# Optimization experiments

Measured on AMD Instinct MI355X. Metric: run time of the kernel, lower is better.

Reference implementation:

```python
import jax, jax.numpy as jnp
import numpy as np

B, S, H = 8, 4096, 2048
E, F, K = 32, 128, 2
UTIL_BONUS = 0.1
CAP_PENALTY = 0.1


def setup_inputs() -> dict:
    key = jax.random.key(0)
    ks = jax.random.split(key, 4)
    hidden = jax.random.normal(ks[0], (B, S, H), dtype=jnp.float32)
    router_w = 0.02 * jax.random.normal(ks[1], (E, H), dtype=jnp.float32)
    router_b = jnp.zeros((E,), dtype=jnp.float32)
    w1 = 0.02 * jax.random.normal(ks[2], (E, F, H), dtype=jnp.float32)
    b1 = jnp.zeros((E, F), dtype=jnp.float32)
    w2 = 0.02 * jax.random.normal(ks[3], (E, H, F), dtype=jnp.float32)
    b2 = jnp.zeros((E, H), dtype=jnp.float32)
    activation_counts = jnp.zeros((E,), dtype=jnp.float32)
    expert_drift = jnp.zeros((E,), dtype=jnp.float32)
    return {"hidden": hidden, "router_w": router_w, "router_b": router_b,
            "w1": w1, "b1": b1, "w2": w2, "b2": b2,
            "activation_counts": activation_counts, "expert_drift": expert_drift}


def reference(hidden, router_w, router_b, w1, b1, w2, b2, activation_counts, expert_drift):
    # --- router with usage bonus / capacity penalty (buffers are zero at init) ---
    pooled = hidden.mean(axis=1)                      # [B, H]
    base_logits = pooled @ router_w.T + router_b      # [B, E]
    total = activation_counts.sum()
    usage = activation_counts / jnp.maximum(total, 1e-8)
    bonus = jnp.where(total > 0.0, UTIL_BONUS * (1.0 - usage), jnp.zeros_like(usage))
    usage_norm = activation_counts / jnp.maximum(activation_counts.max(), 1e-8)
    drift_norm = expert_drift / jnp.maximum(expert_drift.max(), 1e-8)
    penalty = CAP_PENALTY * 0.5 * (usage_norm + drift_norm)
    logits = base_logits + bonus[None, :] - penalty[None, :]
    router_probs = jax.nn.softmax(logits, axis=-1)    # [B, E]

    topk_probs, topk_idx = jax.lax.top_k(router_probs, K)  # [B, K]
    topk_probs = topk_probs / jnp.maximum(topk_probs.sum(axis=-1, keepdims=True), 1e-8)

    # --- gather selected expert weights and apply to the full sequence ---
    W1 = w1[topk_idx]   # [B, K, F, H]
    B1 = b1[topk_idx]   # [B, K, F]
    W2 = w2[topk_idx]   # [B, K, H, F]
    B2 = b2[topk_idx]   # [B, K, H]

    h1 = jnp.einsum('bsh,bkfh->bksf', hidden, W1) + B1[:, :, None, :]
    h1 = jax.nn.gelu(h1, approximate=False)           # torch nn.GELU default = exact erf
    out = jnp.einsum('bksf,bkhf->bksh', h1, W2) + B2[:, :, None, :]
    delta = jnp.einsum('bk,bksh->bsh', topk_probs, out)  # weighted combine
    return delta, topk_idx, topk_probs, router_probs
```

## Files before the change

### kernel.cpp

```cpp
#include <hip/hip_runtime.h>
#include <hip/hip_bf16.h>

#define BB 8
#define SS 4096
#define HH 2048
#define EE 32
#define FF 128

constexpr size_t DELTA_N = (size_t)BB * SS * HH;
constexpr size_t WELEM = (size_t)EE * FF * HH;
constexpr size_t WBYTES = WELEM * 2;
constexpr size_t HB16_BYTES = (size_t)BB * SS * HH * 2;

typedef short bf16x8 __attribute__((ext_vector_type(8)));
typedef float f32x4 __attribute__((ext_vector_type(4)));
typedef unsigned short u16;
typedef __attribute__((address_space(3))) unsigned char as3u8;
typedef __attribute__((address_space(1))) const unsigned char as1u8;

#define WAITV(N)                                             \
  do {                                                       \
    asm volatile("s_waitcnt vmcnt(" #N ")" ::: "memory");    \
    __builtin_amdgcn_sched_barrier(0);                       \
  } while (0)
#define BARRIER()                                            \
  do {                                                       \
    __builtin_amdgcn_s_barrier();                            \
    __builtin_amdgcn_sched_barrier(0);                       \
  } while (0)

__device__ __forceinline__ u16 f2bfu(float x) {
  unsigned int u = __float_as_uint(x);
  u = (u + 0x7FFFu + ((u >> 16) & 1u)) >> 16;
  return (u16)u;
}

__device__ __forceinline__ unsigned int pk2(float a, float b) {
  union { __hip_bfloat162 h; unsigned int u; } c;
  c.h = __float22bfloat162_rn(make_float2(a, b));
  return c.u;
}

__device__ __forceinline__ bf16x8 pack8(float4 a, float4 b) {
  union { bf16x8 v; unsigned int u[4]; } r;
  r.u[0] = pk2(a.x, a.y);
  r.u[1] = pk2(a.z, a.w);
  r.u[2] = pk2(b.x, b.y);
  r.u[3] = pk2(b.z, b.w);
  return r.v;
}

__device__ __forceinline__ void glds16(const void* g, void* l) {
  __builtin_amdgcn_global_load_lds((as1u8*)g, (as3u8*)l, 16, 0, 0);
}

__global__ void k_zero(float* __restrict__ ws, int n) {
  int i = blockIdx.x * 256 + threadIdx.x;
  if (i < n) ws[i] = 0.0f;
}

__global__ void k_pack(const float* __restrict__ w1, const float* __restrict__ w2,
                       u16* __restrict__ w1p, u16* __restrict__ w2p) {
  unsigned c = blockIdx.x * 256 + threadIdx.x;
  const float* src;
  u16* dst;
  if (c < 1048576u) {
    unsigned e = c >> 15, ci = c & 32767u;
    unsigned it = ci >> 10;
    unsigned cb = (ci & 1023u) * 16u;
    unsigned col = cb >> 7;
    unsigned kb = (cb & 127u) ^ ((col & 7u) << 4);
    unsigned k = it * 64u + (kb >> 1);
    src = w1 + ((size_t)(e * 128u + col) * HH + k);
    dst = w1p + (size_t)c * 8;
  } else {
    unsigned c2 = c - 1048576u;
    unsigned e = c2 >> 15, ci = c2 & 32767u;
    unsigned h = ci >> 4;
    unsigned cb = (ci & 15u) * 16u;
    unsigned kb = cb ^ ((h & 7u) << 4);
    unsigned f = kb >> 1;
    src = w2 + ((size_t)(e * 2048u + h) * FF + f);
    dst = w2p + (size_t)c2 * 8;
  }
  float4 a = *(const float4*)src;
  float4 b = *(const float4*)(src + 4);
  *(bf16x8*)dst = pack8(a, b);
}

__global__ __launch_bounds__(512) void k_pooltile(const float* __restrict__ hidden,
                                                  u16* __restrict__ hb16,
                                                  float* __restrict__ psum) {
  const int b  = blockIdx.x >> 6;
  const int st = blockIdx.x & 63;
  const int t  = threadIdx.x;

  const float* src = hidden + ((size_t)b * SS + st * 64) * HH + t * 4;
  char* dbase = (char*)hb16 + (size_t)(b * 64 + st) * 262144 + (size_t)(t >> 4) * 8192;
  const int kq = (t & 15) * 8;

  float4 s = make_float4(0.f, 0.f, 0.f, 0.f);
  for (int r = 0; r < 64; ++r) {
    float4 v = *(const float4*)(src + (size_t)r * HH);
    s.x += v.x; s.y += v.y; s.z += v.z; s.w += v.w;
    *(uint2*)(dbase + r * 128 + (kq ^ ((r & 7) << 4))) =
        make_uint2(pk2(v.x, v.y), pk2(v.z, v.w));
  }
  float* pp = psum + (size_t)b * HH + t * 4;
  atomicAdd(pp + 0, s.x);
  atomicAdd(pp + 1, s.y);
  atomicAdd(pp + 2, s.z);
  atomicAdd(pp + 3, s.w);
}

__global__ void k_logits(const float* __restrict__ psum, const float* __restrict__ rw,
                         float* __restrict__ logits) {
  int b = blockIdx.x >> 5;
  int e = blockIdx.x & 31;
  int tid = threadIdx.x;
  float acc = 0.0f;
  const float* ps = psum + (size_t)b * HH;
  const float* wr = rw + (size_t)e * HH;
  for (int h = tid; h < HH; h += 256) acc = fmaf(ps[h], wr[h], acc);
  __shared__ float red[256];
  red[tid] = acc;
  __syncthreads();
  for (int w = 128; w > 0; w >>= 1) {
    if (tid < w) red[tid] += red[tid + w];
    __syncthreads();
  }
  if (tid == 0) logits[blockIdx.x] = red[0] * (1.0f / (float)SS);
}

__global__ void k_topk(const float* __restrict__ logits, const float* __restrict__ rb,
                       const float* __restrict__ counts, const float* __restrict__ drift,
                       int* __restrict__ sel, float* __restrict__ pscale,
                       float* __restrict__ out) {
  int t = threadIdx.x;
  int b = t >> 5, e = t & 31;
  float total = 0.0f, cmax = 0.0f, dmax = 0.0f;
  for (int i = 0; i < EE; ++i) {
    float c = counts[i]; total += c; cmax = fmaxf(cmax, c);
    float d = drift[i];  dmax = fmaxf(dmax, d);
  }
  float cnt = counts[e], dr = drift[e];
  float usage = cnt / fmaxf(total, 1e-8f);
  float bonus = (total > 0.0f) ? 0.1f * (1.0f - usage) : 0.0f;
  float un = cnt / fmaxf(cmax, 1e-8f);
  float dn = dr / fmaxf(dmax, 1e-8f);
  float l = logits[t] + rb[e] + bonus - 0.05f * (un + dn);

  float m = l;
  for (int w = 16; w; w >>= 1) m = fmaxf(m, __shfl_xor(m, w, 32));
  float p = expf(l - m);
  float ssum = p;
  for (int w = 16; w; w >>= 1) ssum += __shfl_xor(ssum, w, 32);
  float prob = p / ssum;
  out[DELTA_N + 32 + t] = prob;

  float v1 = prob; int i1 = e;
  for (int w = 16; w; w >>= 1) {
    float ov = __shfl_xor(v1, w, 32); int oi = __shfl_xor(i1, w, 32);
    if (ov > v1 || (ov == v1 && oi < i1)) { v1 = ov; i1 = oi; }
  }
  float v2 = (e == i1) ? -1.0f : prob; int i2 = e;
  for (int w = 16; w; w >>= 1) {
    float ov = __shfl_xor(v2, w, 32); int oi = __shfl_xor(i2, w, 32);
    if (ov > v2 || (ov == v2 && oi < i2)) { v2 = ov; i2 = oi; }
  }
  if (e == 0) {
    float denom = fmaxf(v1 + v2, 1e-8f);
    float tp0 = v1 / denom, tp1 = v2 / denom;
    sel[b * 2 + 0] = i1;
    sel[b * 2 + 1] = i2;
    pscale[b * 2 + 0] = tp0;
    pscale[b * 2 + 1] = tp1;
    out[DELTA_N + 0 + b * 2 + 0] = (float)i1;
    out[DELTA_N + 0 + b * 2 + 1] = (float)i2;
    out[DELTA_N + 16 + b * 2 + 0] = tp0;
    out[DELTA_N + 16 + b * 2 + 1] = tp1;
  }
}

__global__ __launch_bounds__(512, 4) void k_ffn2(
    const u16* __restrict__ hb16, const float* __restrict__ bs1,
    const float* __restrict__ bs2, const u16* __restrict__ w1p,
    const u16* __restrict__ w2p, const int* __restrict__ sel,
    const float* __restrict__ pscale, float* __restrict__ out) {
  __shared__ __align__(16) char smem[81920];

  const int t    = threadIdx.x;
  const int lane = t & 63;
  const int wv   = t >> 6;
  const int l15  = lane & 15;
  const int lk   = lane >> 4;

  const int bid = blockIdx.x;
  const int b   = bid & 7;
  const int st  = bid >> 3;

  const int e0 = sel[2 * b], e1 = sel[2 * b + 1];
  const float p0 = pscale[2 * b], p1 = pscale[2 * b + 1];

  const int wr = wv >> 2, wc = wv & 3;
  const int RB = wr * 32, CB = wc * 64;

  const char* hsrc = (const char*)hb16 + (size_t)(b * 64 + st) * 262144 + (size_t)t * 16;
  const size_t eB1 = (size_t)((wv < 4) ? e0 : e1) * 524288;
  const char* bsrc = (const char*)w1p + eB1 + (size_t)(wv & 3) * 4096 + (size_t)lane * 16;

  f32x4 zero = {0.f, 0.f, 0.f, 0.f};
  f32x4 acc1[2][4];
#pragma unroll
  for (int i = 0; i < 2; ++i)
#pragma unroll
    for (int j = 0; j < 4; ++j) acc1[i][j] = zero;

  auto STAGE1 = [&](int bb, int j) {
    glds16(hsrc + (size_t)j * 8192, &smem[bb * 8192 + (size_t)t * 16]);
    const char* s = bsrc + (size_t)j * 16384;
    char* d = &smem[16384 + bb * 32768 + wv * 4096 + lane * 16];
#pragma unroll
    for (int r = 0; r < 4; ++r) glds16(s + r * 1024, d + r * 1024);
  };

  STAGE1(0, 0);
  STAGE1(1, 1);

#pragma unroll 1
  for (int j = 0; j < 32; ++j) {
    if (j < 31) { WAITV(5); } else { WAITV(0); }
    BARRIER();
    const int cb = j & 1;
    const char* sa = &smem[cb * 8192];
    const char* sb = &smem[16384 + cb * 32768];
#pragma unroll
    for (int kk = 0; kk < 2; ++kk) {
      bf16x8 af[2], bv[4];
#pragma unroll
      for (int rt = 0; rt < 2; ++rt) {
        int row = RB + rt * 16 + l15;
        af[rt] = *(const bf16x8*)(sa + row * 128 + ((kk * 64 + lk * 16) ^ ((row & 7) << 4)));
      }
#pragma unroll
      for (int ct = 0; ct < 4; ++ct) {
        int col = CB + ct * 16 + l15;
        bv[ct] = *(const bf16x8*)(sb + col * 128 + ((kk * 64 + lk * 16) ^ ((col & 7) << 4)));
      }
#pragma unroll
      for (int rt = 0; rt < 2; ++rt)
#pragma unroll
        for (int ct = 0; ct < 4; ++ct)
          acc1[rt][ct] = __builtin_amdgcn_mfma_f32_16x16x32_bf16(af[rt], bv[ct], acc1[rt][ct], 0, 0, 0);
    }
    BARRIER();
    if (j < 30) STAGE1(cb, j + 2);
  }

#pragma unroll
  for (int ct = 0; ct < 4; ++ct) {
    int c = CB + ct * 16 + l15;
    int ec = (c < 128) ? e0 : e1;
    float pc = (c < 128) ? p0 : p1;
    float bias = bs1[ec * FF + (c & 127)];
#pragma unroll
    for (int rt = 0; rt < 2; ++rt)
#pragma unroll
      for (int r = 0; r < 4; ++r) {
        int row = RB + rt * 16 + lk * 4 + r;
        float x = acc1[rt][ct][r] + bias;
        float g = 0.5f * x * (1.0f + erff(x * 0.70710678118654752f));
        *(u16*)&smem[row * 512 + ((c * 2) ^ ((row & 7) << 4))] = f2bfu(pc * g);
      }
  }
  __syncthreads();

  const size_t eB2 = (size_t)((wv < 4) ? e0 : e1) * 524288;
  const char* tsrc = (const char*)w2p + eB2 + (size_t)(wv & 3) * 2048 + (size_t)lane * 16;
  auto STAGE2 = [&](int bb, int n) {
    const char* s = tsrc + (size_t)n * 8192;
    char* d = &smem[32768 + bb * 16384 + (wv >> 2) * 8192 + (wv & 3) * 2048 + lane * 16];
    glds16(s, d);
    glds16(s + 1024, d + 1024);
  };
  STAGE2(0, 0);
  STAGE2(1, 1);

  const int wr2 = wv & 3, wc2 = wv >> 2;
  bf16x8 pa[8];
  {
    int row = wr2 * 16 + l15;
    unsigned sw = (row & 7) << 4;
#pragma unroll
    for (int ks = 0; ks < 8; ++ks)
      pa[ks] = *(const bf16x8*)&smem[row * 512 + ((ks * 64 + lk * 16) ^ sw)];
  }

  float* obase = out + ((size_t)b * SS + st * 64) * HH;
  const int hin = wc2 * 16 + l15;

#pragma unroll 1
  for (int n0 = 0; n0 < 64; ++n0) {
    if (n0 == 0) { WAITV(2); }
    else if (n0 == 63) { WAITV(4); }
    else { WAITV(6); }
    BARRIER();
    const int cb = n0 % 3;
    f32x4 acc2 = zero;
    const char* tb = &smem[32768 + cb * 16384];
#pragma unroll
    for (int ks = 0; ks < 8; ++ks) {
      bf16x8 bv = *(const bf16x8*)(tb + (ks >> 2) * 8192 + hin * 256 +
                                   (((ks & 3) * 64 + lk * 16) ^ ((hin & 7) << 4)));
      acc2 = __builtin_amdgcn_mfma_f32_16x16x32_bf16(pa[ks], bv, acc2, 0, 0, 0);
    }
    const int h = n0 * 32 + hin;
    float bias = p0 * bs2[(size_t)e0 * HH + h] + p1 * bs2[(size_t)e1 * HH + h];
#pragma unroll
    for (int r = 0; r < 4; ++r) {
      int row = wr2 * 16 + lk * 4 + r;
      obase[(size_t)row * HH + h] = acc2[r] + bias;
    }
    if (n0 < 62) STAGE2((n0 + 2) % 3, n0 + 2);
  }
}

__global__ void k_pool_logits(const float* __restrict__ hidden,
                              const float* __restrict__ rw,
                              float* __restrict__ logits) {
  const int b  = blockIdx.x >> 6;
  const int hc = (blockIdx.x >> 3) & 7;
  const int sq = blockIdx.x & 7;
  const int t  = threadIdx.x;
  const int tx = t & 63;
  const int qq = t >> 6;
  const int h0 = hc * 256;

  const float* p = hidden + ((size_t)b * SS + sq * 512 + qq * 128) * HH + h0 + tx * 4;
  float4 s = make_float4(0.f, 0.f, 0.f, 0.f);
  for (int i = 0; i < 128; ++i) {
    float4 v = *(const float4*)(p + (size_t)i * HH);
    s.x += v.x; s.y += v.y; s.z += v.z; s.w += v.w;
  }
  __shared__ float ps[4][256];
  __shared__ float pl[256];
  *(float4*)&ps[qq][tx * 4] = s;
  __syncthreads();
  pl[t] = ps[0][t] + ps[1][t] + ps[2][t] + ps[3][t];
  __syncthreads();

  const int e = t >> 3, part = t & 7;
  const float* wrp = rw + (size_t)e * HH + h0 + part * 32;
  float v = 0.f;
#pragma unroll
  for (int m = 0; m < 32; ++m) v += pl[part * 32 + m] * wrp[m];
  v += __shfl_xor(v, 1, 8);
  v += __shfl_xor(v, 2, 8);
  v += __shfl_xor(v, 4, 8);
  if (part == 0) atomicAdd(&logits[b * EE + e], v * (1.0f / (float)SS));
}

__global__ __launch_bounds__(512, 2) void k_ffn_fb(
    const float* __restrict__ hidden, const float* __restrict__ w1,
    const float* __restrict__ b1, const float* __restrict__ w2,
    const float* __restrict__ b2, const int* __restrict__ sel,
    const float* __restrict__ pscale, float* __restrict__ out) {
  __shared__ unsigned char sA[2][64 * 128];
  __shared__ unsigned char sG[64 * 512];

  const int t    = threadIdx.x;
  const int lane = t & 63;
  const int wv   = t >> 6;
  const int wr   = wv >> 2;
  const int wc   = wv & 3;
  const int l15  = lane & 15;
  const int lk   = lane >> 4;

  const int bid = blockIdx.x;
  const int b   = bid & 7;
  const int s0  = (bid >> 3) * 64;

  const int e0 = sel[2 * b], e1 = sel[2 * b + 1];
  const float p0 = pscale[2 * b], p1 = pscale[2 * b + 1];

  const float* hbase = hidden + ((size_t)b * SS + s0) * HH;
  const int srow = t >> 4;
  const int skq  = t & 15;

  float4 R[2];
  const float* wp[4];
#pragma unroll
  for (int ct = 0; ct < 4; ++ct) {
    int cbase = wc * 64 + ct * 16;
    int ec = (cbase < 128) ? e0 : e1;
    int f  = (cbase & 127) + l15;
    wp[ct] = w1 + ((size_t)ec * FF + f) * HH + lk * 8;
  }

  f32x4 zero = {0.f, 0.f, 0.f, 0.f};
  f32x4 acc1[2][4];
#pragma unroll
  for (int i = 0; i < 2; ++i)
#pragma unroll
    for (int j = 0; j < 4; ++j) acc1[i][j] = zero;

#pragma unroll
  for (int p = 0; p < 2; ++p)
    R[p] = *(const float4*)(hbase + (size_t)(srow + 32 * p) * HH + skq * 4);
#pragma unroll
  for (int p = 0; p < 2; ++p) {
    int row = srow + 32 * p;
    int addr = row * 128 + ((skq * 8) ^ ((row & 7) << 4));
    *(uint2*)(&sA[0][addr]) = make_uint2(pk2(R[p].x, R[p].y), pk2(R[p].z, R[p].w));
  }
  __syncthreads();

  for (int it = 0; it < 32; ++it) {
    const int buf = it & 1;
    if (it < 31) {
      const int k0 = (it + 1) * 64;
#pragma unroll
      for (int p = 0; p < 2; ++p)
        R[p] = *(const float4*)(hbase + (size_t)(srow + 32 * p) * HH + k0 + skq * 4);
    }
#pragma unroll
    for (int kk = 0; kk < 2; ++kk) {
      bf16x8 a[2];
#pragma unroll
      for (int rt = 0; rt < 2; ++rt) {
        int row = wr * 32 + rt * 16 + l15;
        a[rt] = *(const bf16x8*)(&sA[buf][row * 128 + ((kk * 64 + lk * 16) ^ ((row & 7) << 4))]);
      }
#pragma unroll
      for (int ct = 0; ct < 4; ++ct) {
        const float* q = wp[ct] + it * 64 + kk * 32;
        bf16x8 bfr = pack8(*(const float4*)q, *(const float4*)(q + 4));
#pragma unroll
        for (int rt = 0; rt < 2; ++rt)
          acc1[rt][ct] = __builtin_amdgcn_mfma_f32_16x16x32_bf16(a[rt], bfr, acc1[rt][ct], 0, 0, 0);
      }
    }
    if (it < 31) {
#pragma unroll
      for (int p = 0; p < 2; ++p) {
        int row = srow + 32 * p;
        int addr = row * 128 + ((skq * 8) ^ ((row & 7) << 4));
        *(uint2*)(&sA[buf ^ 1][addr]) = make_uint2(pk2(R[p].x, R[p].y), pk2(R[p].z, R[p].w));
      }
    }
    __syncthreads();
  }

#pragma unroll
  for (int ct = 0; ct < 4; ++ct) {
    int c = wc * 64 + ct * 16 + l15;
    int ec = (c < 128) ? e0 : e1;
    float pc = (c < 128) ? p0 : p1;
    float bias = b1[ec * FF + (c & 127)];
#pragma unroll
    for (int rt = 0; rt < 2; ++rt)
#pragma unroll
      for (int r = 0; r < 4; ++r) {
        int row = wr * 32 + rt * 16 + lk * 4 + r;
        float x = acc1[rt][ct][r] + bias;
        float g = 0.5f * x * (1.0f + erff(x * 0.70710678118654752f));
        int addr = row * 512 + ((c * 2) ^ ((row & 7) << 4));
        *(u16*)(&sG[addr]) = f2bfu(pc * g);
      }
  }
  __syncthreads();

  bf16x8 pa[2][8];
#pragma unroll
  for (int rt = 0; rt < 2; ++rt) {
    int row = wr * 32 + rt * 16 + l15;
#pragma unroll
    for (int ks = 0; ks < 8; ++ks)
      pa[rt][ks] = *(const bf16x8*)(&sG[row * 512 + ((ks * 64 + lk * 16) ^ ((row & 7) << 4))]);
  }

  float* obase = out + ((size_t)b * SS + s0) * HH;
  for (int ct = 0; ct < 32; ++ct) {
    const int h = wc * 512 + ct * 16 + l15;
    f32x4 acc[2];
    acc[0] = zero; acc[1] = zero;
    const float* q0 = w2 + ((size_t)e0 * HH + h) * FF + lk * 8;
    const float* q1 = w2 + ((size_t)e1 * HH + h) * FF + lk * 8;
#pragma unroll
    for (int ks = 0; ks < 8; ++ks) {
      const float* q = (ks < 4 ? q0 : q1) + (ks & 3) * 32;
      bf16x8 bfr = pack8(*(const float4*)q, *(const float4*)(q + 4));
#pragma unroll
      for (int rt = 0; rt < 2; ++rt)
        acc[rt] = __builtin_amdgcn_mfma_f32_16x16x32_bf16(pa[rt][ks], bfr, acc[rt], 0, 0, 0);
    }
    float bias = p0 * b2[(size_t)e0 * HH + h] + p1 * b2[(size_t)e1 * HH + h];
#pragma unroll
    for (int rt = 0; rt < 2; ++rt)
#pragma unroll
      for (int r = 0; r < 4; ++r) {
        int row = wr * 32 + rt * 16 + lk * 4 + r;
        obase[(size_t)row * HH + h] = acc[rt][r] + bias;
      }
  }
}

extern "C" void kernel_launch(void* const* d_in, const int* in_sizes, int n_in,
                              void* d_out, int out_size, void* d_ws, size_t ws_size,
                              hipStream_t stream) {
  const float* hidden   = (const float*)d_in[0];
  const float* router_w = (const float*)d_in[1];
  const float* router_b = (const float*)d_in[2];
  const float* w1       = (const float*)d_in[3];
  const float* b1       = (const float*)d_in[4];
  const float* w2       = (const float*)d_in[5];
  const float* b2       = (const float*)d_in[6];
  const float* counts   = (const float*)d_in[7];
  const float* drift    = (const float*)d_in[8];
  float* out            = (float*)d_out;

  float* logits = (float*)d_ws;
  int*   sel    = (int*)((char*)d_ws + 1024);
  float* pscale = (float*)((char*)d_ws + 1088);
  float* psum   = (float*)((char*)d_ws + 4096);

  const size_t need_big = 131072 + 2 * WBYTES + HB16_BYTES;

  if (ws_size >= need_big) {
    u16* w1p  = (u16*)((char*)d_ws + 131072);
    u16* w2p  = (u16*)((char*)d_ws + 131072 + WBYTES);
    u16* hb16 = (u16*)((char*)d_ws + 131072 + 2 * WBYTES);
    k_zero<<<68, 256, 0, stream>>>(logits, 17408);
    k_pack<<<8192, 256, 0, stream>>>(w1, w2, w1p, w2p);
    k_pooltile<<<512, 512, 0, stream>>>(hidden, hb16, psum);
    k_logits<<<256, 256, 0, stream>>>(psum, router_w, logits);
    k_topk<<<1, 256, 0, stream>>>(logits, router_b, counts, drift, sel, pscale, out);
    k_ffn2<<<512, 512, 0, stream>>>(hb16, b1, b2, w1p, w2p, sel, pscale, out);
  } else {
    k_zero<<<2, 256, 0, stream>>>(logits, 288);
    k_pool_logits<<<512, 256, 0, stream>>>(hidden, router_w, logits);
    k_topk<<<1, 256, 0, stream>>>(logits, router_b, counts, drift, sel, pscale, out);
    k_ffn_fb<<<512, 512, 0, stream>>>(hidden, w1, b1, w2, b2, sel, pscale, out);
  }
}
```

Before: 279.1 us.

## Double FFN row tile to 128 tokens per block and restage W2 loads

The fused FFN kernel now handles 128 sequence rows per block instead of 64, with 256 blocks instead of 512. Each block streams its selected experts' W1 and W2 slices once for twice as many tokens, halving weight traffic per token. The second GEMM now uses 64-column W2 tiles with double buffering, preloaded bias values and a wider accumulator per wave. The cost is more LDS (128 KB) and registers, which lowers occupancy to 2 blocks per CU and leaves fewer blocks to spread across the GPU.

```diff
diff --git a/kernel.cpp b/kernel.cpp
--- a/kernel.cpp
+++ b/kernel.cpp
@@ -182,12 +182,12 @@
   }
 }
 
-__global__ __launch_bounds__(512, 4) void k_ffn2(
+__global__ __launch_bounds__(512, 2) void k_ffn4(
     const u16* __restrict__ hb16, const float* __restrict__ bs1,
     const float* __restrict__ bs2, const u16* __restrict__ w1p,
     const u16* __restrict__ w2p, const int* __restrict__ sel,
     const float* __restrict__ pscale, float* __restrict__ out) {
-  __shared__ __align__(16) char smem[81920];
+  __shared__ __align__(16) char smem[131072];
 
   const int t    = threadIdx.x;
   const int lane = t & 63;
@@ -203,23 +203,26 @@
   const float p0 = pscale[2 * b], p1 = pscale[2 * b + 1];
 
   const int wr = wv >> 2, wc = wv & 3;
-  const int RB = wr * 32, CB = wc * 64;
-
-  const char* hsrc = (const char*)hb16 + (size_t)(b * 64 + st) * 262144 + (size_t)t * 16;
+  const int RB = wr * 64, CB = wc * 64;
+
+  const char* hsrcA = (const char*)hb16 + (size_t)(b * 64 + st * 2) * 262144;
   const size_t eB1 = (size_t)((wv < 4) ? e0 : e1) * 524288;
   const char* bsrc = (const char*)w1p + eB1 + (size_t)(wv & 3) * 4096 + (size_t)lane * 16;
 
   f32x4 zero = {0.f, 0.f, 0.f, 0.f};
-  f32x4 acc1[2][4];
-#pragma unroll
-  for (int i = 0; i < 2; ++i)
+  f32x4 acc1[4][4];
+#pragma unroll
+  for (int i = 0; i < 4; ++i)
 #pragma unroll
     for (int j = 0; j < 4; ++j) acc1[i][j] = zero;
 
   auto STAGE1 = [&](int bb, int j) {
-    glds16(hsrc + (size_t)j * 8192, &smem[bb * 8192 + (size_t)t * 16]);
+    glds16(hsrcA + (size_t)j * 8192 + (size_t)t * 16,
+           &smem[bb * 16384 + (size_t)t * 16]);
+    glds16(hsrcA + 262144 + (size_t)j * 8192 + (size_t)t * 16,
+           &smem[bb * 16384 + 8192 + (size_t)t * 16]);
     const char* s = bsrc + (size_t)j * 16384;
-    char* d = &smem[16384 + bb * 32768 + wv * 4096 + lane * 16];
+    char* d = &smem[32768 + bb * 32768 + wv * 4096 + lane * 16];
 #pragma unroll
     for (int r = 0; r < 4; ++r) glds16(s + r * 1024, d + r * 1024);
   };
@@ -229,32 +232,35 @@
 
 #pragma unroll 1
   for (int j = 0; j < 32; ++j) {
-    if (j < 31) { WAITV(5); } else { WAITV(0); }
+    if (j < 31) { WAITV(6); } else { WAITV(0); }
     BARRIER();
     const int cb = j & 1;
-    const char* sa = &smem[cb * 8192];
-    const char* sb = &smem[16384 + cb * 32768];
+    const char* sa = &smem[cb * 16384];
+    const char* sb = &smem[32768 + cb * 32768];
 #pragma unroll
     for (int kk = 0; kk < 2; ++kk) {
-      bf16x8 af[2], bv[4];
-#pragma unroll
-      for (int rt = 0; rt < 2; ++rt) {
+      bf16x8 af[4], bv[4];
+#pragma unroll
+      for (int rt = 0; rt < 4; ++rt) {
         int row = RB + rt * 16 + l15;
-        af[rt] = *(const bf16x8*)(sa + row * 128 + ((kk * 64 + lk * 16) ^ ((row & 7) << 4)));
+        int sub = row >> 6, r64 = row & 63;
+        af[rt] = *(const bf16x8*)(sa + sub * 8192 + r64 * 128 +
+                                  ((kk * 64 + lk * 16) ^ ((r64 & 7) << 4)));
       }
 #pragma unroll
       for (int ct = 0; ct < 4; ++ct) {
         int col = CB + ct * 16 + l15;
-        bv[ct] = *(const bf16x8*)(sb + col * 128 + ((kk * 64 + lk * 16) ^ ((col & 7) << 4)));
-      }
-#pragma unroll
-      for (int rt = 0; rt < 2; ++rt)
+        bv[ct] = *(const bf16x8*)(sb + col * 128 +
+                                  ((kk * 64 + lk * 16) ^ ((col & 7) << 4)));
+      }
+#pragma unroll
+      for (int rt = 0; rt < 4; ++rt)
 #pragma unroll
         for (int ct = 0; ct < 4; ++ct)
           acc1[rt][ct] = __builtin_amdgcn_mfma_f32_16x16x32_bf16(af[rt], bv[ct], acc1[rt][ct], 0, 0, 0);
     }
     BARRIER();
-    if (j < 30) STAGE1(cb, j + 2);
+    if (j < 30) STAGE1(j & 1, j + 2);
   }
 
 #pragma unroll
@@ -264,7 +270,7 @@
     float pc = (c < 128) ? p0 : p1;
     float bias = bs1[ec * FF + (c & 127)];
 #pragma unroll
-    for (int rt = 0; rt < 2; ++rt)
+    for (int rt = 0; rt < 4; ++rt)
 #pragma unroll
       for (int r = 0; r < 4; ++r) {
         int row = RB + rt * 16 + lk * 4 + r;
@@ -273,55 +279,75 @@
         *(u16*)&smem[row * 512 + ((c * 2) ^ ((row & 7) << 4))] = f2bfu(pc * g);
       }
   }
-  __syncthreads();
-
-  const size_t eB2 = (size_t)((wv < 4) ? e0 : e1) * 524288;
-  const char* tsrc = (const char*)w2p + eB2 + (size_t)(wv & 3) * 2048 + (size_t)lane * 16;
+
+  const char* w2c0 = (const char*)w2p + (size_t)e0 * 524288;
+  const char* w2c1 = (const char*)w2p + (size_t)e1 * 524288;
+  const char* wsel = (lane & 16) ? w2c1 : w2c0;
+  const int hh_l = wv * 8 + (lane >> 5);
+  const int inb  = (lane & 15) * 16;
   auto STAGE2 = [&](int bb, int n) {
-    const char* s = tsrc + (size_t)n * 8192;
-    char* d = &smem[32768 + bb * 16384 + (wv >> 2) * 8192 + (wv & 3) * 2048 + lane * 16];
-    glds16(s, d);
-    glds16(s + 1024, d + 1024);
+    char* d = &smem[65536 + bb * 32768 + wv * 4096 + lane * 16];
+#pragma unroll
+    for (int i = 0; i < 4; ++i)
+      glds16(wsel + (size_t)(n * 64 + hh_l + i * 2) * 256 + inb, d + i * 1024);
   };
   STAGE2(0, 0);
   STAGE2(1, 1);
 
-  const int wr2 = wv & 3, wc2 = wv >> 2;
-  bf16x8 pa[8];
-  {
-    int row = wr2 * 16 + l15;
+  const int wr2 = wv & 1, wc2 = wv >> 1;
+  const int colf = wc2 * 16 + l15;
+  float cb0 = bs2[(size_t)e0 * HH + colf];
+  float cb1 = bs2[(size_t)e1 * HH + colf];
+
+  __syncthreads();
+
+  bf16x8 pa[4][8];
+#pragma unroll
+  for (int rt = 0; rt < 4; ++rt) {
+    int row = wr2 * 64 + rt * 16 + l15;
     unsigned sw = (row & 7) << 4;
 #pragma unroll
     for (int ks = 0; ks < 8; ++ks)
-      pa[ks] = *(const bf16x8*)&smem[row * 512 + ((ks * 64 + lk * 16) ^ sw)];
-  }
-
-  float* obase = out + ((size_t)b * SS + st * 64) * HH;
-  const int hin = wc2 * 16 + l15;
+      pa[rt][ks] = *(const bf16x8*)&smem[row * 512 + ((ks * 64 + lk * 16) ^ sw)];
+  }
+
+  float* obase = out + ((size_t)b * SS + st * 128) * HH;
 
 #pragma unroll 1
-  for (int n0 = 0; n0 < 64; ++n0) {
-    if (n0 == 0) { WAITV(2); }
-    else if (n0 == 63) { WAITV(4); }
-    else { WAITV(6); }
+  for (int n0 = 0; n0 < 32; ++n0) {
+    WAITV(4);
     BARRIER();
-    const int cb = n0 % 3;
-    f32x4 acc2 = zero;
-    const char* tb = &smem[32768 + cb * 16384];
+    float nb0 = 0.f, nb1 = 0.f;
+    if (n0 < 31) {
+      nb0 = bs2[(size_t)e0 * HH + (n0 + 1) * 64 + colf];
+      nb1 = bs2[(size_t)e1 * HH + (n0 + 1) * 64 + colf];
+    }
+    const int cb2 = n0 & 1;
+    const char* tb = &smem[65536 + cb2 * 32768];
+    f32x4 acc2[4];
+#pragma unroll
+    for (int i = 0; i < 4; ++i) acc2[i] = zero;
 #pragma unroll
     for (int ks = 0; ks < 8; ++ks) {
-      bf16x8 bv = *(const bf16x8*)(tb + (ks >> 2) * 8192 + hin * 256 +
-                                   (((ks & 3) * 64 + lk * 16) ^ ((hin & 7) << 4)));
-      acc2 = __builtin_amdgcn_mfma_f32_16x16x32_bf16(pa[ks], bv, acc2, 0, 0, 0);
-    }
-    const int h = n0 * 32 + hin;
-    float bias = p0 * bs2[(size_t)e0 * HH + h] + p1 * bs2[(size_t)e1 * HH + h];
-#pragma unroll
-    for (int r = 0; r < 4; ++r) {
-      int row = wr2 * 16 + lk * 4 + r;
-      obase[(size_t)row * HH + h] = acc2[r] + bias;
-    }
-    if (n0 < 62) STAGE2((n0 + 2) % 3, n0 + 2);
+      bf16x8 bv = *(const bf16x8*)(tb + colf * 512 + (ks >> 2) * 256 +
+                                   (((ks & 3) * 64 + lk * 16) ^ ((colf & 7) << 4)));
+#pragma unroll
+      for (int rt = 0; rt < 4; ++rt)
+        acc2[rt] = __builtin_amdgcn_mfma_f32_16x16x32_bf16(pa[rt][ks], bv, acc2[rt], 0, 0, 0);
+    }
+    BARRIER();
+    float bias = p0 * cb0 + p1 * cb1;
+    const int col = n0 * 64 + colf;
+#pragma unroll
+    for (int rt = 0; rt < 4; ++rt)
+#pragma unroll
+      for (int r = 0; r < 4; ++r) {
+        int row = wr2 * 64 + rt * 16 + lk * 4 + r;
+        obase[(size_t)row * HH + col] = acc2[rt][r] + bias;
+      }
+    cb0 = nb0;
+    cb1 = nb1;
+    if (n0 < 30) STAGE2(n0 & 1, n0 + 2);
   }
 }
 
@@ -535,7 +561,7 @@
     k_pooltile<<<512, 512, 0, stream>>>(hidden, hb16, psum);
     k_logits<<<256, 256, 0, stream>>>(psum, router_w, logits);
     k_topk<<<1, 256, 0, stream>>>(logits, router_b, counts, drift, sel, pscale, out);
-    k_ffn2<<<512, 512, 0, stream>>>(hb16, b1, b2, w1p, w2p, sel, pscale, out);
+    k_ffn4<<<256, 512, 0, stream>>>(hb16, b1, b2, w1p, w2p, sel, pscale, out);
   } else {
     k_zero<<<2, 256, 0, stream>>>(logits, 288);
     k_pool_logits<<<512, 256, 0, stream>>>(hidden, router_w, logits);
```

New measurement: 304.2 us. 9.0% more time.

## Merge pool and weight-pack kernels; widen FFN stage-2 tile to reuse weights

Applied to the files above, without the earlier changes.

Fuses the hidden-state pooling/bf16 tiling kernel and the expert weight packing kernel into one launch, with the pack work spread over extra blocks. This removes a launch and lets both memory-bound jobs run at the same time. In the FFN kernel, stage 2 now has each wave compute two 16-row tiles per loaded W2 fragment, using 64-column chunks with double buffering instead of 32-column triple buffering. It also precomputes the probability-weighted bias into shared memory, cutting iterations and redundant global bias loads. The cost is more registers for the A fragments and a larger shared-memory layout.

```diff
diff --git a/kernel.cpp b/kernel.cpp
--- a/kernel.cpp
+++ b/kernel.cpp
@@ -59,58 +59,61 @@
   if (i < n) ws[i] = 0.0f;
 }
 
-__global__ void k_pack(const float* __restrict__ w1, const float* __restrict__ w2,
-                       u16* __restrict__ w1p, u16* __restrict__ w2p) {
-  unsigned c = blockIdx.x * 256 + threadIdx.x;
-  const float* src;
-  u16* dst;
-  if (c < 1048576u) {
-    unsigned e = c >> 15, ci = c & 32767u;
-    unsigned it = ci >> 10;
-    unsigned cb = (ci & 1023u) * 16u;
-    unsigned col = cb >> 7;
-    unsigned kb = (cb & 127u) ^ ((col & 7u) << 4);
-    unsigned k = it * 64u + (kb >> 1);
-    src = w1 + ((size_t)(e * 128u + col) * HH + k);
-    dst = w1p + (size_t)c * 8;
+__global__ __launch_bounds__(512) void k_poolpack(
+    const float* __restrict__ hidden, const float* __restrict__ w1,
+    const float* __restrict__ w2, u16* __restrict__ hb16,
+    float* __restrict__ psum, u16* __restrict__ w1p, u16* __restrict__ w2p) {
+  const int bid = blockIdx.x;
+  const int t = threadIdx.x;
+  if (bid < 512) {
+    const int b  = bid >> 6;
+    const int st = bid & 63;
+    const float* src = hidden + ((size_t)b * SS + st * 64) * HH + t * 4;
+    char* dbase = (char*)hb16 + (size_t)(b * 64 + st) * 262144 + (size_t)(t >> 4) * 8192;
+    const int kq = (t & 15) * 8;
+    float4 s = make_float4(0.f, 0.f, 0.f, 0.f);
+    for (int r = 0; r < 64; ++r) {
+      float4 v = *(const float4*)(src + (size_t)r * HH);
+      s.x += v.x; s.y += v.y; s.z += v.z; s.w += v.w;
+      *(uint2*)(dbase + r * 128 + (kq ^ ((r & 7) << 4))) =
+          make_uint2(pk2(v.x, v.y), pk2(v.z, v.w));
+    }
+    float* pp = psum + (size_t)b * HH + t * 4;
+    atomicAdd(pp + 0, s.x);
+    atomicAdd(pp + 1, s.y);
+    atomicAdd(pp + 2, s.z);
+    atomicAdd(pp + 3, s.w);
   } else {
-    unsigned c2 = c - 1048576u;
-    unsigned e = c2 >> 15, ci = c2 & 32767u;
-    unsigned h = ci >> 4;
-    unsigned cb = (ci & 15u) * 16u;
-    unsigned kb = cb ^ ((h & 7u) << 4);
-    unsigned f = kb >> 1;
-    src = w2 + ((size_t)(e * 2048u + h) * FF + f);
-    dst = w2p + (size_t)c2 * 8;
-  }
-  float4 a = *(const float4*)src;
-  float4 b = *(const float4*)(src + 4);
-  *(bf16x8*)dst = pack8(a, b);
-}
-
-__global__ __launch_bounds__(512) void k_pooltile(const float* __restrict__ hidden,
-                                                  u16* __restrict__ hb16,
-                                                  float* __restrict__ psum) {
-  const int b  = blockIdx.x >> 6;
-  const int st = blockIdx.x & 63;
-  const int t  = threadIdx.x;
-
-  const float* src = hidden + ((size_t)b * SS + st * 64) * HH + t * 4;
-  char* dbase = (char*)hb16 + (size_t)(b * 64 + st) * 262144 + (size_t)(t >> 4) * 8192;
-  const int kq = (t & 15) * 8;
-
-  float4 s = make_float4(0.f, 0.f, 0.f, 0.f);
-  for (int r = 0; r < 64; ++r) {
-    float4 v = *(const float4*)(src + (size_t)r * HH);
-    s.x += v.x; s.y += v.y; s.z += v.z; s.w += v.w;
-    *(uint2*)(dbase + r * 128 + (kq ^ ((r & 7) << 4))) =
-        make_uint2(pk2(v.x, v.y), pk2(v.z, v.w));
-  }
-  float* pp = psum + (size_t)b * HH + t * 4;
-  atomicAdd(pp + 0, s.x);
-  atomicAdd(pp + 1, s.y);
-  atomicAdd(pp + 2, s.z);
-  atomicAdd(pp + 3, s.w);
+    const int pb = bid - 512;
+#pragma unroll 1
+    for (int i = 0; i < 8; ++i) {
+      unsigned c = (unsigned)pb * 4096u + (unsigned)i * 512u + (unsigned)t;
+      const float* src;
+      u16* dst;
+      if (c < 1048576u) {
+        unsigned e = c >> 15, ci = c & 32767u;
+        unsigned it = ci >> 10;
+        unsigned cb = (ci & 1023u) * 16u;
+        unsigned col = cb >> 7;
+        unsigned kb = (cb & 127u) ^ ((col & 7u) << 4);
+        unsigned k = it * 64u + (kb >> 1);
+        src = w1 + ((size_t)(e * 128u + col) * HH + k);
+        dst = w1p + (size_t)c * 8;
+      } else {
+        unsigned c2 = c - 1048576u;
+        unsigned e = c2 >> 15, ci = c2 & 32767u;
+        unsigned h = ci >> 4;
+        unsigned cb = (ci & 15u) * 16u;
+        unsigned kb = cb ^ ((h & 7u) << 4);
+        unsigned f = kb >> 1;
+        src = w2 + ((size_t)(e * 2048u + h) * FF + f);
+        dst = w2p + (size_t)c2 * 8;
+      }
+      float4 a = *(const float4*)src;
+      float4 b2v = *(const float4*)(src + 4);
+      *(bf16x8*)dst = pack8(a, b2v);
+    }
+  }
 }
 
 __global__ void k_logits(const float* __restrict__ psum, const float* __restrict__ rw,
@@ -182,7 +185,7 @@
   }
 }
 
-__global__ __launch_bounds__(512, 4) void k_ffn2(
+__global__ __launch_bounds__(512, 4) void k_ffn5(
     const u16* __restrict__ hb16, const float* __restrict__ bs1,
     const float* __restrict__ bs2, const u16* __restrict__ w1p,
     const u16* __restrict__ w2p, const int* __restrict__ sel,
@@ -217,9 +220,9 @@
     for (int j = 0; j < 4; ++j) acc1[i][j] = zero;
 
   auto STAGE1 = [&](int bb, int j) {
-    glds16(hsrc + (size_t)j * 8192, &smem[bb * 8192 + (size_t)t * 16]);
+    glds16(hsrc + (size_t)j * 8192, &smem[65536 + bb * 8192 + (size_t)t * 16]);
     const char* s = bsrc + (size_t)j * 16384;
-    char* d = &smem[16384 + bb * 32768 + wv * 4096 + lane * 16];
+    char* d = &smem[bb * 32768 + wv * 4096 + lane * 16];
 #pragma unroll
     for (int r = 0; r < 4; ++r) glds16(s + r * 1024, d + r * 1024);
   };
@@ -232,8 +235,8 @@
     if (j < 31) { WAITV(5); } else { WAITV(0); }
     BARRIER();
     const int cb = j & 1;
-    const char* sa = &smem[cb * 8192];
-    const char* sb = &smem[16384 + cb * 32768];
+    const char* sa = &smem[65536 + cb * 8192];
+    const char* sb = &smem[cb * 32768];
 #pragma unroll
     for (int kk = 0; kk < 2; ++kk) {
       bf16x8 af[2], bv[4];
@@ -254,7 +257,7 @@
           acc1[rt][ct] = __builtin_amdgcn_mfma_f32_16x16x32_bf16(af[rt], bv[ct], acc1[rt][ct], 0, 0, 0);
     }
     BARRIER();
-    if (j < 30) STAGE1(cb, j + 2);
+    if (j < 30) STAGE1(j & 1, j + 2);
   }
 
 #pragma unroll
@@ -273,55 +276,71 @@
         *(u16*)&smem[row * 512 + ((c * 2) ^ ((row & 7) << 4))] = f2bfu(pc * g);
       }
   }
+  {
+    float4 q0 = *(const float4*)(bs2 + (size_t)e0 * HH + t * 4);
+    float4 q1 = *(const float4*)(bs2 + (size_t)e1 * HH + t * 4);
+    float4 bb;
+    bb.x = p0 * q0.x + p1 * q1.x;
+    bb.y = p0 * q0.y + p1 * q1.y;
+    bb.z = p0 * q0.z + p1 * q1.z;
+    bb.w = p0 * q0.w + p1 * q1.w;
+    *(float4*)&smem[65536 + t * 16] = bb;
+  }
   __syncthreads();
 
-  const size_t eB2 = (size_t)((wv < 4) ? e0 : e1) * 524288;
-  const char* tsrc = (const char*)w2p + eB2 + (size_t)(wv & 3) * 2048 + (size_t)lane * 16;
+  const int wr2 = wv >> 2, wc2 = wv & 3;
+  bf16x8 pa[2][8];
+#pragma unroll
+  for (int rt = 0; rt < 2; ++rt) {
+    int row = wr2 * 32 + rt * 16 + l15;
+    unsigned sw = (row & 7) << 4;
+#pragma unroll
+    for (int ks = 0; ks < 8; ++ks)
+      pa[rt][ks] = *(const bf16x8*)&smem[row * 512 + ((ks * 64 + lk * 16) ^ sw)];
+  }
+  BARRIER();
+
+  const char* wse = (const char*)w2p + (size_t)((wv < 4) ? e0 : e1) * 524288;
   auto STAGE2 = [&](int bb, int n) {
-    const char* s = tsrc + (size_t)n * 8192;
-    char* d = &smem[32768 + bb * 16384 + (wv >> 2) * 8192 + (wv & 3) * 2048 + lane * 16];
-    glds16(s, d);
-    glds16(s + 1024, d + 1024);
+    const char* s = wse + (size_t)(n * 64 + (wv & 3) * 16) * 256 + (size_t)lane * 16;
+    char* d = &smem[bb * 32768 + (wv >> 2) * 16384 + (wv & 3) * 4096 + lane * 16];
+#pragma unroll
+    for (int i = 0; i < 4; ++i) glds16(s + i * 1024, d + i * 1024);
   };
   STAGE2(0, 0);
   STAGE2(1, 1);
 
-  const int wr2 = wv & 3, wc2 = wv >> 2;
-  bf16x8 pa[8];
-  {
-    int row = wr2 * 16 + l15;
-    unsigned sw = (row & 7) << 4;
-#pragma unroll
-    for (int ks = 0; ks < 8; ++ks)
-      pa[ks] = *(const bf16x8*)&smem[row * 512 + ((ks * 64 + lk * 16) ^ sw)];
-  }
-
   float* obase = out + ((size_t)b * SS + st * 64) * HH;
-  const int hin = wc2 * 16 + l15;
+  const int h64 = wc2 * 16 + l15;
 
 #pragma unroll 1
-  for (int n0 = 0; n0 < 64; ++n0) {
-    if (n0 == 0) { WAITV(2); }
-    else if (n0 == 63) { WAITV(4); }
-    else { WAITV(6); }
+  for (int n0 = 0; n0 < 32; ++n0) {
+    if (n0 == 0) { WAITV(4); }
+    else if (n0 == 31) { WAITV(8); }
+    else { WAITV(12); }
     BARRIER();
-    const int cb = n0 % 3;
-    f32x4 acc2 = zero;
-    const char* tb = &smem[32768 + cb * 16384];
+    const char* tb = &smem[(n0 & 1) * 32768];
+    float bias = *(const float*)&smem[65536 + (n0 * 64 + h64) * 4];
+    f32x4 acc2[2];
+    acc2[0] = zero; acc2[1] = zero;
 #pragma unroll
     for (int ks = 0; ks < 8; ++ks) {
-      bf16x8 bv = *(const bf16x8*)(tb + (ks >> 2) * 8192 + hin * 256 +
-                                   (((ks & 3) * 64 + lk * 16) ^ ((hin & 7) << 4)));
-      acc2 = __builtin_amdgcn_mfma_f32_16x16x32_bf16(pa[ks], bv, acc2, 0, 0, 0);
-    }
-    const int h = n0 * 32 + hin;
-    float bias = p0 * bs2[(size_t)e0 * HH + h] + p1 * bs2[(size_t)e1 * HH + h];
-#pragma unroll
-    for (int r = 0; r < 4; ++r) {
-      int row = wr2 * 16 + lk * 4 + r;
-      obase[(size_t)row * HH + h] = acc2[r] + bias;
-    }
-    if (n0 < 62) STAGE2((n0 + 2) % 3, n0 + 2);
+      bf16x8 bv = *(const bf16x8*)(tb + (ks >> 2) * 16384 + h64 * 256 +
+                                   (((ks & 3) * 64 + lk * 16) ^ ((h64 & 7) << 4)));
+#pragma unroll
+      for (int rt = 0; rt < 2; ++rt)
+        acc2[rt] = __builtin_amdgcn_mfma_f32_16x16x32_bf16(pa[rt][ks], bv, acc2[rt], 0, 0, 0);
+    }
+    BARRIER();
+    const int col = n0 * 64 + h64;
+#pragma unroll
+    for (int rt = 0; rt < 2; ++rt)
+#pragma unroll
+      for (int r = 0; r < 4; ++r) {
+        int row = wr2 * 32 + rt * 16 + lk * 4 + r;
+        obase[(size_t)row * HH + col] = acc2[rt][r] + bias;
+      }
+    if (n0 < 30) STAGE2(n0 & 1, n0 + 2);
   }
 }
 
@@ -531,11 +550,10 @@
     u16* w2p  = (u16*)((char*)d_ws + 131072 + WBYTES);
     u16* hb16 = (u16*)((char*)d_ws + 131072 + 2 * WBYTES);
     k_zero<<<68, 256, 0, stream>>>(logits, 17408);
-    k_pack<<<8192, 256, 0, stream>>>(w1, w2, w1p, w2p);
-    k_pooltile<<<512, 512, 0, stream>>>(hidden, hb16, psum);
+    k_poolpack<<<1024, 512, 0, stream>>>(hidden, w1, w2, hb16, psum, w1p, w2p);
     k_logits<<<256, 256, 0, stream>>>(psum, router_w, logits);
     k_topk<<<1, 256, 0, stream>>>(logits, router_b, counts, drift, sel, pscale, out);
-    k_ffn2<<<512, 512, 0, stream>>>(hb16, b1, b2, w1p, w2p, sel, pscale, out);
+    k_ffn5<<<512, 512, 0, stream>>>(hb16, b1, b2, w1p, w2p, sel, pscale, out);
   } else {
     k_zero<<<2, 256, 0, stream>>>(logits, 288);
     k_pool_logits<<<512, 256, 0, stream>>>(hidden, router_w, logits);
```

Measured after the change: 260.9 us (median of 2 runs). -6.5%, faster.
